# Optimization experiments

Hardware: AMD Instinct MI355X
Metric: run time of the kernel (lower is better)

## Reference

```python
import jax, jax.numpy as jnp
import numpy as np

B, L, D, P = 4, 128, 256, 1024
TU, TB = 86400, 3600  # tu = 24*3600, time_bin = 3600
NEG = float(-2**32 + 1)


def setup_inputs() -> dict:
    key = jax.random.key(0)
    ks = jax.random.split(key, 16)
    src = jax.random.normal(ks[0], (B, L, D), jnp.float32)
    batch_seq_lens = jax.random.randint(ks[1], (B,), L // 2, L + 1, dtype=jnp.int32)
    ts = jnp.sort(jax.random.randint(ks[2], (B, L), 0, 864000, dtype=jnp.int32), axis=1)
    lts = ts + jax.random.randint(ks[3], (B, L), 0, 7200, dtype=jnp.int32)
    s = 0.02
    hour_emb = (jax.random.normal(ks[4], (TU // TB + 2, D), jnp.float32) * s).at[0].set(0.0)  # padding_idx=0
    day_emb = (jax.random.normal(ks[5], (8, D), jnp.float32) * s).at[0].set(0.0)              # padding_idx=0
    wq = jax.random.normal(ks[6], (D, D), jnp.float32) * s
    wk = jax.random.normal(ks[7], (D, D), jnp.float32) * s
    wv = jax.random.normal(ks[8], (D, D), jnp.float32) * s
    wf1 = jax.random.normal(ks[9], (D, D), jnp.float32) * s
    wf2 = jax.random.normal(ks[10], (D, D), jnp.float32) * s
    wdec = jax.random.uniform(ks[11], (P, D), jnp.float32, -0.1, 0.1)  # init_weights uniform(-0.1,0.1)
    z = jnp.zeros((D,), jnp.float32)
    return {
        'src': src, 'hour_emb': hour_emb, 'day_emb': day_emb,
        'wq': wq, 'bq': z, 'wk': wk, 'bk': z, 'wv': wv, 'bv': z,
        'g11': jnp.ones((D,), jnp.float32), 'b11': z,
        'wf1': wf1, 'bf1': z, 'wf2': wf2, 'bf2': z,
        'g12': jnp.ones((D,), jnp.float32), 'b12': z,
        'wdec': wdec, 'bdec': jnp.zeros((P,), jnp.float32),
        'batch_seq_lens': batch_seq_lens,
        'batch_input_seqs_ts': ts,
        'batch_label_seqs_ts': lts,
    }


def _ln(x, g, b):
    m = jnp.mean(x, axis=-1, keepdims=True)
    v = jnp.var(x, axis=-1, keepdims=True)
    return (x - m) * jax.lax.rsqrt(v + 1e-5) * g + b


def reference(src, hour_emb, day_emb, wq, bq, wk, bk, wv, bv, g11, b11,
              wf1, bf1, wf2, bf2, g12, b12, wdec, bdec,
              batch_seq_lens, batch_input_seqs_ts, batch_label_seqs_ts):
    ts, lts = batch_input_seqs_ts, batch_label_seqs_ts
    # per-pair time intervals, [B,L,L]
    diff = ts[:, :, None] - ts[:, None, :]
    hour = (diff % TU) // TB + 2
    # faithful to source: 'if i == j' compares batch index to row position
    hour = jnp.where((jnp.arange(B)[:, None] == jnp.arange(L)[None, :])[:, :, None], 1, hour)
    day = jnp.minimum(diff // TU + 1, 7)
    ldiff = lts[:, :, None] - ts[:, None, :]
    lhour = (ldiff % TU) // TB + 2
    lday = jnp.minimum(ldiff // TU + 1, 7)
    tril = jnp.tril(jnp.ones((L, L), bool))
    rows_valid = jnp.arange(L)[None, :] < batch_seq_lens[:, None]  # [B,L]
    valid = tril[None] & rows_valid[:, :, None]
    # index 0 == padding row (zero embedding), matching zeros-init + padding_idx=0
    hour = jnp.where(valid, hour, 0)
    day = jnp.where(valid, day, 0)
    lhour = jnp.where(valid, lhour, 0)
    lday = jnp.where(valid, lday, 0)
    hE = hour_emb[hour]    # [B,L,L,D]
    dE = day_emb[day]
    lhE = hour_emb[lhour]
    ldE = day_emb[lday]

    Q = src @ wq.T + bq
    K = src @ wk.T + bk
    V = src @ wv.T + bv
    aw = (jnp.einsum('bjd,bkd->bjk', Q, K)
          + jnp.einsum('bjkd,bjd->bjk', hE, Q)
          + jnp.einsum('bjkd,bjd->bjk', dE, Q)) / jnp.sqrt(jnp.float32(D))
    mask = (~tril)[None] | (~rows_valid)[:, :, None]
    aw = jnp.where(mask, NEG, aw)
    aw = jax.nn.softmax(aw, axis=-1)
    x = (jnp.einsum('bjk,bkd->bjd', aw, V)
         + jnp.einsum('bjk,bjkd->bjd', aw, hE)
         + jnp.einsum('bjk,bjkd->bjd', aw, dE))
    x = _ln(x + src, g11, b11)
    f = jnp.maximum(x @ wf1.T + bf1, 0.0) @ wf2.T + bf2  # dropout is identity at eval
    f = _ln(x + f, g12, b12)

    # out4[b,j,k,:] = f[b,k,:] + label interval embeddings
    out4 = f[:, None, :, :] + lhE + ldE            # [B,L,L,D]
    dec = out4 @ wdec.T + bdec                     # [B,L,L,P]
    counts = jnp.arange(1, L + 1, dtype=dec.dtype)
    pooled = jnp.einsum('bjkp,jk->bjp', dec, tril.astype(dec.dtype)) / counts[None, :, None]
    return pooled
```

## Files before the change

### kernel.cpp

```cpp
#include <hip/hip_runtime.h>
#include <hip/hip_bf16.h>

#define LL 128
#define DD 256
#define PP 1024
#define TU_C 86400
#define TB_C 3600
#define NEGF -4294967296.0f

#define FMA4(ACC_, SS_, WW_) { (ACC_).x += (SS_)*(WW_).x; (ACC_).y += (SS_)*(WW_).y; (ACC_).z += (SS_)*(WW_).z; (ACC_).w += (SS_)*(WW_).w; }
#define ADD4(ACC_, WW_) { (ACC_).x += (WW_).x; (ACC_).y += (WW_).y; (ACC_).z += (WW_).z; (ACC_).w += (WW_).w; }

__device__ __forceinline__ float wredSum(float v) {
#pragma unroll
  for (int o = 32; o; o >>= 1) v += __shfl_xor(v, o);
  return v;
}
__device__ __forceinline__ float wredMax(float v) {
#pragma unroll
  for (int o = 32; o; o >>= 1) v = fmaxf(v, __shfl_xor(v, o));
  return v;
}

__global__ __launch_bounds__(256) void k_wt(
    const float* __restrict__ wq, const float* __restrict__ wk,
    const float* __restrict__ wv, const float* __restrict__ wf1,
    const float* __restrict__ wf2, const float* __restrict__ wdec,
    float* __restrict__ wt)
{
  __shared__ float s[32][33];
  const int tile = blockIdx.x;
  const float* src; float* dst; int R, m;
  if (tile < 320) {
    const int mi = tile >> 6; m = tile & 63;
    src = (mi == 0) ? wq : (mi == 1) ? wk : (mi == 2) ? wv : (mi == 3) ? wf1 : wf2;
    dst = wt + mi * 65536; R = 256;
  } else {
    m = tile - 320; src = wdec; dst = wt + 327680; R = 1024;
  }
  const int sr = (m >> 3) * 32, sc0 = (m & 7) * 32;
  const int tx = threadIdx.x & 31, ty = threadIdx.x >> 5;
#pragma unroll
  for (int i = 0; i < 4; ++i)
    s[ty + 8 * i][tx] = src[(sr + ty + 8 * i) * 256 + sc0 + tx];
  __syncthreads();
#pragma unroll
  for (int i = 0; i < 4; ++i)
    dst[(sc0 + ty + 8 * i) * R + sr + tx] = s[tx][ty + 8 * i];
}

__global__ __launch_bounds__(256) void k_qkv(
    const float* __restrict__ src, const float* __restrict__ wt,
    const float* __restrict__ bq, const float* __restrict__ bk,
    const float* __restrict__ bv,
    float* __restrict__ Q, float* __restrict__ KT, float* __restrict__ V)
{
  __shared__ float xs[8][DD];
  __shared__ float ps[4][8][DD];
  const int t = threadIdx.x, l = t & 63, w = t >> 6;
  const int r0 = blockIdx.x * 8;
  const int mat = blockIdx.y;
  const float* wm = wt + mat * 65536;
  for (int i = t; i < 8 * DD; i += 256) xs[i >> 8][i & 255] = src[r0 * DD + i];
  __syncthreads();
  const int col = 4 * l;
  float4 acc[8];
#pragma unroll
  for (int r = 0; r < 8; ++r) acc[r] = (float4){0.f, 0.f, 0.f, 0.f};
  const int e0 = 64 * w;
  for (int e = e0; e < e0 + 64; e += 4) {
    float4 xr[8];
#pragma unroll
    for (int r = 0; r < 8; ++r) xr[r] = *(const float4*)&xs[r][e];
#pragma unroll
    for (int c = 0; c < 4; ++c) {
      const float4 w4 = *(const float4*)(wm + (e + c) * DD + col);
#pragma unroll
      for (int r = 0; r < 8; ++r) {
        const float xv = (c == 0) ? xr[r].x : (c == 1) ? xr[r].y : (c == 2) ? xr[r].z : xr[r].w;
        FMA4(acc[r], xv, w4)
      }
    }
  }
#pragma unroll
  for (int r = 0; r < 8; ++r) *(float4*)&ps[w][r][col] = acc[r];
  __syncthreads();
  const float* bi = (mat == 0) ? bq : (mat == 1) ? bk : bv;
#pragma unroll
  for (int g = 0; g < 2; ++g) {
    const int combo = g * 256 + t;
    const int r = combo >> 6, cgp = combo & 63;
    const int c4 = 4 * cgp;
    float4 o = *(const float4*)(bi + c4);
    ADD4(o, (*(const float4*)&ps[0][r][c4]))
    ADD4(o, (*(const float4*)&ps[1][r][c4]))
    ADD4(o, (*(const float4*)&ps[2][r][c4]))
    ADD4(o, (*(const float4*)&ps[3][r][c4]))
    const int rr = r0 + r;
    if (mat == 1) {
      const int bA = rr >> 7, kA = rr & 127;
      KT[bA * 32768 + (c4 + 0) * 128 + kA] = o.x;
      KT[bA * 32768 + (c4 + 1) * 128 + kA] = o.y;
      KT[bA * 32768 + (c4 + 2) * 128 + kA] = o.z;
      KT[bA * 32768 + (c4 + 3) * 128 + kA] = o.w;
    } else {
      float* op = (mat == 0) ? Q : V;
      *(float4*)(op + rr * DD + c4) = o;
    }
  }
}

__global__ __launch_bounds__(512) void k_attn(
    const float* __restrict__ Q, const float* __restrict__ KT,
    const float* __restrict__ Vm, const float* __restrict__ src,
    const float* __restrict__ hour_emb, const float* __restrict__ day_emb,
    const int* __restrict__ seq_lens, const int* __restrict__ ts_g,
    const float* __restrict__ g11, const float* __restrict__ b11,
    const float* __restrict__ wt1, const float* __restrict__ bf1,
    const float* __restrict__ wt2, const float* __restrict__ bf2,
    const float* __restrict__ g12, const float* __restrict__ b12,
    float* __restrict__ F)
{
  const int b = blockIdx.x >> 6;
  const int j0 = (blockIdx.x & 63) * 2;
  const int t = threadIdx.x, w = t >> 6, l = t & 63;
  const int col = 4 * l;
  __shared__ float qs[2][DD];
  __shared__ int   tsl[LL];
  __shared__ float qhd[2][34];
  __shared__ float whd[2][34];
  __shared__ float red[8];
  __shared__ float ss[2][LL];
  __shared__ float xs2[2][DD];
  __shared__ float hs2[2][DD];
  __shared__ float ps[8][2][DD];
  const int row0 = b * LL + j0;
  qs[t >> 8][t & 255] = Q[row0 * DD + t];
  if (t < LL) tsl[t] = ts_g[b * LL + t];
  if (t < 68) whd[t / 34][t % 34] = 0.f;
  __syncthreads();
  float kdot = 0.f;
  int krow = 0, kidx = 0;
  if (w < 4) {
    krow = w >> 1;
    kidx = ((w & 1) << 6) | l;
    const float* ktb = KT + b * 32768;
    float4 kd = {0.f,0.f,0.f,0.f};
#pragma unroll 8
    for (int e = 0; e < DD; e += 4) {
      const float4 q4 = *(const float4*)&qs[krow][e];
      const float* kp = ktb + e * LL + kidx;
      kd.x += q4.x * kp[0];
      kd.y += q4.y * kp[128];
      kd.z += q4.z * kp[256];
      kd.w += q4.w * kp[384];
    }
    kdot = (kd.x + kd.y) + (kd.z + kd.w);
  } else if (w < 6 && l < 34) {
    const int r = w - 4;
    const float* ep = (l < 26) ? (hour_emb + l * DD) : (day_emb + (l - 26) * DD);
    float4 ed = {0.f,0.f,0.f,0.f};
    for (int e = 0; e < DD; e += 4) {
      const float4 q4 = *(const float4*)&qs[r][e];
      const float4 e4 = *(const float4*)(ep + e);
      ed.x += q4.x * e4.x; ed.y += q4.y * e4.y;
      ed.z += q4.z * e4.z; ed.w += q4.w * e4.w;
    }
    qhd[r][l] = (ed.x + ed.y) + (ed.z + ed.w);
  }
  __syncthreads();
  const int len = seq_lens[b];
  float s = NEGF;
  int hidx = 0, didx = 0;
  if (w < 4) {
    const int jrow = j0 + krow;
    if (kidx <= jrow && jrow < len) {
      const int df = tsl[jrow] - tsl[kidx];
      hidx = (jrow == b) ? 1 : ((df % TU_C) / TB_C + 2);
      didx = min(df / TU_C + 1, 7);
      s = (kdot + qhd[krow][hidx] + qhd[krow][26 + didx]) * 0.0625f;
    }
    const float mv = wredMax(s);
    if (l == 0) red[w] = mv;
  }
  __syncthreads();
  float p = 0.f;
  if (w < 4) {
    const float m = fmaxf(red[2 * krow], red[2 * krow + 1]);
    p = expf(s - m);
    const float sv = wredSum(p);
    if (l == 0) red[4 + w] = sv;
  }
  __syncthreads();
  if (w < 4) {
    const float Z = red[4 + 2 * krow] + red[5 + 2 * krow];
    const float aw = p / Z;
    ss[krow][kidx] = aw;
    atomicAdd(&whd[krow][hidx], aw);
    atomicAdd(&whd[krow][26 + didx], aw);
  }
  __syncthreads();
  {
    float4 a0 = {0.f,0.f,0.f,0.f}, a1 = {0.f,0.f,0.f,0.f};
    const float* vb = Vm + b * LL * DD + col;
    const int k0 = 16 * w;
#pragma unroll
    for (int kk = 0; kk < 16; ++kk) {
      const int k = k0 + kk;
      const float4 v4 = *(const float4*)(vb + k * DD);
      FMA4(a0, ss[0][k], v4)
      FMA4(a1, ss[1][k], v4)
    }
    if (w == 0) {
#pragma unroll
      for (int i = 0; i < 26; ++i)
        FMA4(a0, whd[0][i], *(const float4*)(hour_emb + i * DD + col))
    } else if (w == 1) {
#pragma unroll
      for (int i = 0; i < 26; ++i)
        FMA4(a1, whd[1][i], *(const float4*)(hour_emb + i * DD + col))
    } else if (w == 2) {
#pragma unroll
      for (int i = 0; i < 8; ++i)
        FMA4(a0, whd[0][26 + i], *(const float4*)(day_emb + i * DD + col))
      const float4 s4 = *(const float4*)(src + row0 * DD + col);
      ADD4(a0, s4)
    } else if (w == 3) {
#pragma unroll
      for (int i = 0; i < 8; ++i)
        FMA4(a1, whd[1][26 + i], *(const float4*)(day_emb + i * DD + col))
      const float4 s4 = *(const float4*)(src + (row0 + 1) * DD + col);
      ADD4(a1, s4)
    }
    *(float4*)&ps[w][0][col] = a0;
    *(float4*)&ps[w][1][col] = a1;
  }
  __syncthreads();
  if (w < 2) {
    float4 x = *(const float4*)&ps[0][w][col];
#pragma unroll
    for (int i = 1; i < 8; ++i) ADD4(x, (*(const float4*)&ps[i][w][col]))
    const float sm = wredSum(x.x + x.y + x.z + x.w);
    const float sq = wredSum(x.x*x.x + x.y*x.y + x.z*x.z + x.w*x.w);
    const float mean = sm * (1.f / DD);
    const float rstd = rsqrtf(sq * (1.f / DD) - mean * mean + 1e-5f);
    const float4 g4 = *(const float4*)(g11 + col);
    const float4 b4 = *(const float4*)(b11 + col);
    x.x = (x.x - mean) * rstd * g4.x + b4.x;
    x.y = (x.y - mean) * rstd * g4.y + b4.y;
    x.z = (x.z - mean) * rstd * g4.z + b4.z;
    x.w = (x.w - mean) * rstd * g4.w + b4.w;
    *(float4*)&xs2[w][col] = x;
  }
  __syncthreads();
  {
    float4 a0 = {0.f,0.f,0.f,0.f}, a1 = {0.f,0.f,0.f,0.f};
    const int e0 = 32 * w;
#pragma unroll 8
    for (int ee = 0; ee < 32; ++ee) {
      const int e = e0 + ee;
      const float4 w4 = *(const float4*)(wt1 + e * DD + col);
      FMA4(a0, xs2[0][e], w4)
      FMA4(a1, xs2[1][e], w4)
    }
    *(float4*)&ps[w][0][col] = a0;
    *(float4*)&ps[w][1][col] = a1;
  }
  __syncthreads();
  if (w < 2) {
    float4 h = *(const float4*)(bf1 + col);
#pragma unroll
    for (int i = 0; i < 8; ++i) ADD4(h, (*(const float4*)&ps[i][w][col]))
    h.x = fmaxf(h.x, 0.f); h.y = fmaxf(h.y, 0.f);
    h.z = fmaxf(h.z, 0.f); h.w = fmaxf(h.w, 0.f);
    *(float4*)&hs2[w][col] = h;
  }
  __syncthreads();
  {
    float4 a0 = {0.f,0.f,0.f,0.f}, a1 = {0.f,0.f,0.f,0.f};
    const int e0 = 32 * w;
#pragma unroll 8
    for (int ee = 0; ee < 32; ++ee) {
      const int e = e0 + ee;
      const float4 w4 = *(const float4*)(wt2 + e * DD + col);
      FMA4(a0, hs2[0][e], w4)
      FMA4(a1, hs2[1][e], w4)
    }
    *(float4*)&ps[w][0][col] = a0;
    *(float4*)&ps[w][1][col] = a1;
  }
  __syncthreads();
  if (w < 2) {
    float4 o = *(const float4*)(bf2 + col);
#pragma unroll
    for (int i = 0; i < 8; ++i) ADD4(o, (*(const float4*)&ps[i][w][col]))
    const float4 xr = *(const float4*)&xs2[w][col];
    ADD4(o, xr)
    const float sm = wredSum(o.x + o.y + o.z + o.w);
    const float sq = wredSum(o.x*o.x + o.y*o.y + o.z*o.z + o.w*o.w);
    const float mean = sm * (1.f / DD);
    const float rstd = rsqrtf(sq * (1.f / DD) - mean * mean + 1e-5f);
    const float4 g4 = *(const float4*)(g12 + col);
    const float4 b4 = *(const float4*)(b12 + col);
    o.x = (o.x - mean) * rstd * g4.x + b4.x;
    o.y = (o.y - mean) * rstd * g4.y + b4.y;
    o.z = (o.z - mean) * rstd * g4.z + b4.z;
    o.w = (o.w - mean) * rstd * g4.w + b4.w;
    *(float4*)(F + (row0 + w) * DD + col) = o;
  }
}

__global__ __launch_bounds__(256) void k_decf(
    const float* __restrict__ F,
    const float* __restrict__ hour_emb, const float* __restrict__ day_emb,
    const int* __restrict__ seq_lens, const int* __restrict__ ts_g,
    const int* __restrict__ lts_g,
    const float* __restrict__ wtd, const float* __restrict__ bdec,
    float* __restrict__ out)
{
  const int c0 = blockIdx.x * 256;
  const int r0g = blockIdx.y * 8;
  const int b = r0g >> 7, j0 = r0g & 127;
  const int t = threadIdx.x, l = t & 63, w = t >> 6;
  __shared__ float xs[8][DD];
  __shared__ float cnt[8][34];
  __shared__ float ps[4][8][DD];
  for (int i = t; i < 8 * 34; i += 256) (&cnt[0][0])[i] = 0.f;
  __syncthreads();
  const int len = seq_lens[b];
  const int* ts = ts_g + b * LL;
  const int* lts = lts_g + b * LL;
#pragma unroll
  for (int p = 0; p < 4; ++p) {
    const int idx = p * 256 + t;
    const int jj = idx >> 7, k = idx & 127, j = j0 + jj;
    if (k <= j && j < len) {
      const int ld = lts[j] - ts[k];
      atomicAdd(&cnt[jj][(ld % TU_C) / TB_C + 2], 1.f);
      atomicAdd(&cnt[jj][26 + min(ld / TU_C + 1, 7)], 1.f);
    }
  }
  __syncthreads();
  {
    float he[26], de[8];
#pragma unroll
    for (int i = 0; i < 26; ++i) he[i] = hour_emb[i * DD + t];
#pragma unroll
    for (int i = 0; i < 8; ++i)  de[i] = day_emb[i * DD + t];
    const float* fb = F + b * LL * DD + t;
    float A0 = 0.f, A1 = 0.f, A2 = 0.f, A3 = 0.f;
#pragma unroll 4
    for (int k = 0; k < j0; k += 4) {
      A0 += fb[(k + 0) * DD]; A1 += fb[(k + 1) * DD];
      A2 += fb[(k + 2) * DD]; A3 += fb[(k + 3) * DD];
    }
    float gacc = (A0 + A1) + (A2 + A3);
#pragma unroll
    for (int jj = 0; jj < 8; ++jj) {
      gacc += fb[(j0 + jj) * DD];
      float s0 = 0.f, s1 = 0.f;
#pragma unroll
      for (int i = 0; i < 26; i += 2) {
        s0 += cnt[jj][i] * he[i]; s1 += cnt[jj][i + 1] * he[i + 1];
      }
#pragma unroll
      for (int i = 0; i < 8; i += 2) {
        s0 += cnt[jj][26 + i] * de[i]; s1 += cnt[jj][27 + i] * de[i + 1];
      }
      xs[jj][t] = (gacc + s0 + s1) / (float)(j0 + jj + 1);
    }
  }
  __syncthreads();
  const int col = c0 + 4 * l;
  float4 acc[8];
#pragma unroll
  for (int r = 0; r < 8; ++r) acc[r] = (float4){0.f, 0.f, 0.f, 0.f};
  const int e0 = 64 * w;
  for (int e = e0; e < e0 + 64; e += 4) {
    float4 xr[8];
#pragma unroll
    for (int r = 0; r < 8; ++r) xr[r] = *(const float4*)&xs[r][e];
#pragma unroll
    for (int c = 0; c < 4; ++c) {
      const float4 w4 = *(const float4*)(wtd + (e + c) * PP + col);
#pragma unroll
      for (int r = 0; r < 8; ++r) {
        const float xv = (c == 0) ? xr[r].x : (c == 1) ? xr[r].y : (c == 2) ? xr[r].z : xr[r].w;
        FMA4(acc[r], xv, w4)
      }
    }
  }
#pragma unroll
  for (int r = 0; r < 8; ++r) *(float4*)&ps[w][r][4 * l] = acc[r];
  __syncthreads();
#pragma unroll
  for (int g = 0; g < 2; ++g) {
    const int combo = g * 256 + t;
    const int r = combo >> 6, cgp = combo & 63;
    const int c4 = 4 * cgp;
    float4 o = *(const float4*)(bdec + c0 + c4);
    ADD4(o, (*(const float4*)&ps[0][r][c4]))
    ADD4(o, (*(const float4*)&ps[1][r][c4]))
    ADD4(o, (*(const float4*)&ps[2][r][c4]))
    ADD4(o, (*(const float4*)&ps[3][r][c4]))
    *(float4*)(out + (r0g + r) * PP + c0 + c4) = o;
  }
}

extern "C" void kernel_launch(void* const* d_in, const int* in_sizes, int n_in,
                              void* d_out, int out_size, void* d_ws, size_t ws_size,
                              hipStream_t stream)
{
  (void)in_sizes; (void)n_in; (void)out_size; (void)ws_size;
  const float* src      = (const float*)d_in[0];
  const float* hour_emb = (const float*)d_in[1];
  const float* day_emb  = (const float*)d_in[2];
  const float* wq  = (const float*)d_in[3];
  const float* bq  = (const float*)d_in[4];
  const float* wk  = (const float*)d_in[5];
  const float* bk  = (const float*)d_in[6];
  const float* wv  = (const float*)d_in[7];
  const float* bv  = (const float*)d_in[8];
  const float* g11 = (const float*)d_in[9];
  const float* b11 = (const float*)d_in[10];
  const float* wf1 = (const float*)d_in[11];
  const float* bf1 = (const float*)d_in[12];
  const float* wf2 = (const float*)d_in[13];
  const float* bf2 = (const float*)d_in[14];
  const float* g12 = (const float*)d_in[15];
  const float* b12 = (const float*)d_in[16];
  const float* wdec = (const float*)d_in[17];
  const float* bdec = (const float*)d_in[18];
  const int* seq_lens = (const int*)d_in[19];
  const int* ts  = (const int*)d_in[20];
  const int* lts = (const int*)d_in[21];
  float* out = (float*)d_out;
  float* ws = (float*)d_ws;
  float* WT = ws;
  float* Q  = ws + 589824;
  float* KT = ws + 720896;
  float* V  = ws + 851968;
  float* F  = ws + 983040;

  k_wt  <<<576, 256, 0, stream>>>(wq, wk, wv, wf1, wf2, wdec, WT);
  k_qkv <<<dim3(64, 3), 256, 0, stream>>>(src, WT, bq, bk, bv, Q, KT, V);
  k_attn<<<256, 512, 0, stream>>>(Q, KT, V, src, hour_emb, day_emb, seq_lens, ts,
                                  g11, b11, WT + 196608, bf1, WT + 262144, bf2,
                                  g12, b12, F);
  k_decf<<<dim3(4, 64), 256, 0, stream>>>(F, hour_emb, day_emb, seq_lens, ts, lts,
                                          WT + 327680, bdec, out);
}
```

Before: 50.36 us.

## Merge four kernel launches into one cooperative persistent kernel with grid syncs

Replaces the four separate launches (weight transpose, QKV projection, attention+FFN, decoder pooling) with a single cooperative kernel of 256 blocks × 512 threads. The phases are separated by grid.sync() and share one shared-memory union. The goal is to remove per-launch overhead and inter-kernel gaps. Trade-offs: grid-wide barriers have their own cost, some phases now run on fewer or reshaped blocks (QKV uses 192 blocks with 8 waves splitting K), and the larger union shared footprint may reduce occupancy.

Measured after the change: 152.4 us. +202.6%, slower.

```diff
diff --git a/kernel.cpp b/kernel.cpp
--- a/kernel.cpp
+++ b/kernel.cpp
@@ -1,5 +1,8 @@
 #include <hip/hip_runtime.h>
+#include <hip/hip_cooperative_groups.h>
 #include <hip/hip_bf16.h>
+
+namespace cg = cooperative_groups;
 
 #define LL 128
 #define DD 256
@@ -22,81 +25,117 @@
   return v;
 }
 
-__global__ __launch_bounds__(256) void k_wt(
+struct P0S { float tile[2][32][33]; };
+struct P1S { float xs[8][DD]; float ps[4][8][DD]; };
+struct P2S { float qs[2][DD]; int tsl[LL]; float qhd[2][34]; float whd[2][34];
+             float red[8]; float ss[2][LL]; float xs2[2][DD]; float hs2[2][DD];
+             float ps[8][2][DD]; };
+struct P3S { float xs[8][DD]; float cnt[8][34]; float pa[2][DD]; float ps[4][8][DD]; };
+union SMEM { P0S p0; P1S p1; P2S p2; P3S p3; };
+
+__global__ __launch_bounds__(512) void k_mono(
     const float* __restrict__ wq, const float* __restrict__ wk,
     const float* __restrict__ wv, const float* __restrict__ wf1,
     const float* __restrict__ wf2, const float* __restrict__ wdec,
-    float* __restrict__ wt)
-{
-  __shared__ float s[32][33];
-  const int tile = blockIdx.x;
-  const float* src; float* dst; int R, m;
-  if (tile < 320) {
-    const int mi = tile >> 6; m = tile & 63;
-    src = (mi == 0) ? wq : (mi == 1) ? wk : (mi == 2) ? wv : (mi == 3) ? wf1 : wf2;
-    dst = wt + mi * 65536; R = 256;
-  } else {
-    m = tile - 320; src = wdec; dst = wt + 327680; R = 1024;
-  }
-  const int sr = (m >> 3) * 32, sc0 = (m & 7) * 32;
-  const int tx = threadIdx.x & 31, ty = threadIdx.x >> 5;
-#pragma unroll
-  for (int i = 0; i < 4; ++i)
-    s[ty + 8 * i][tx] = src[(sr + ty + 8 * i) * 256 + sc0 + tx];
-  __syncthreads();
-#pragma unroll
-  for (int i = 0; i < 4; ++i)
-    dst[(sc0 + ty + 8 * i) * R + sr + tx] = s[tx][ty + 8 * i];
-}
-
-__global__ __launch_bounds__(256) void k_qkv(
-    const float* __restrict__ src, const float* __restrict__ wt,
+    const float* __restrict__ src,
+    const float* __restrict__ hour_emb, const float* __restrict__ day_emb,
     const float* __restrict__ bq, const float* __restrict__ bk,
     const float* __restrict__ bv,
-    float* __restrict__ Q, float* __restrict__ KT, float* __restrict__ V)
+    const float* __restrict__ g11, const float* __restrict__ b11,
+    const float* __restrict__ bf1, const float* __restrict__ bf2,
+    const float* __restrict__ g12, const float* __restrict__ b12,
+    const float* __restrict__ bdec,
+    const int* __restrict__ seq_lens, const int* __restrict__ ts_g,
+    const int* __restrict__ lts_g,
+    float* __restrict__ out,
+    float* __restrict__ WT, float* __restrict__ Q, float* __restrict__ KT,
+    float* __restrict__ V, float* __restrict__ F)
 {
-  __shared__ float xs[8][DD];
-  __shared__ float ps[4][8][DD];
-  const int t = threadIdx.x, l = t & 63, w = t >> 6;
-  const int r0 = blockIdx.x * 8;
-  const int mat = blockIdx.y;
-  const float* wm = wt + mat * 65536;
-  for (int i = t; i < 8 * DD; i += 256) xs[i >> 8][i & 255] = src[r0 * DD + i];
-  __syncthreads();
-  const int col = 4 * l;
-  float4 acc[8];
-#pragma unroll
-  for (int r = 0; r < 8; ++r) acc[r] = (float4){0.f, 0.f, 0.f, 0.f};
-  const int e0 = 64 * w;
-  for (int e = e0; e < e0 + 64; e += 4) {
-    float4 xr[8];
-#pragma unroll
-    for (int r = 0; r < 8; ++r) xr[r] = *(const float4*)&xs[r][e];
-#pragma unroll
-    for (int c = 0; c < 4; ++c) {
-      const float4 w4 = *(const float4*)(wm + (e + c) * DD + col);
-#pragma unroll
-      for (int r = 0; r < 8; ++r) {
-        const float xv = (c == 0) ? xr[r].x : (c == 1) ? xr[r].y : (c == 2) ? xr[r].z : xr[r].w;
-        FMA4(acc[r], xv, w4)
+  cg::grid_group grid = cg::this_grid();
+  __shared__ SMEM sm;
+  const int bx = blockIdx.x;
+  const int t = threadIdx.x;
+  const int w = t >> 6, l = t & 63;
+
+  {
+    const int sub = t >> 8, tt = t & 255;
+    const int tx = tt & 31, ty = tt >> 5;
+    for (int base = 0; base < 576; base += 512) {
+      const int tile = base + 2 * bx + sub;
+      __syncthreads();
+      const float* sw = nullptr; float* dst = nullptr; int R = 256, m = 0;
+      if (tile < 576) {
+        if (tile < 320) {
+          const int mi = tile >> 6; m = tile & 63;
+          sw = (mi == 0) ? wq : (mi == 1) ? wk : (mi == 2) ? wv : (mi == 3) ? wf1 : wf2;
+          dst = WT + mi * 65536; R = 256;
+        } else {
+          m = tile - 320; sw = wdec; dst = WT + 327680; R = 1024;
+        }
+        const int sr = (m >> 3) * 32, sc0 = (m & 7) * 32;
+#pragma unroll
+        for (int i = 0; i < 4; ++i)
+          sm.p0.tile[sub][ty + 8 * i][tx] = sw[(sr + ty + 8 * i) * 256 + sc0 + tx];
+      }
+      __syncthreads();
+      if (tile < 576) {
+        const int sr = (m >> 3) * 32, sc0 = (m & 7) * 32;
+#pragma unroll
+        for (int i = 0; i < 4; ++i)
+          dst[(sc0 + ty + 8 * i) * R + sr + tx] = sm.p0.tile[sub][tx][ty + 8 * i];
       }
     }
   }
-#pragma unroll
-  for (int r = 0; r < 8; ++r) *(float4*)&ps[w][r][col] = acc[r];
-  __syncthreads();
-  const float* bi = (mat == 0) ? bq : (mat == 1) ? bk : bv;
-#pragma unroll
-  for (int g = 0; g < 2; ++g) {
-    const int combo = g * 256 + t;
-    const int r = combo >> 6, cgp = combo & 63;
-    const int c4 = 4 * cgp;
+  grid.sync();
+
+  if (bx < 192) {
+    const int mat = bx >> 6;
+    const int r0 = (bx & 63) * 8;
+    for (int i = t; i < 8 * DD; i += 512) sm.p1.xs[i >> 8][i & 255] = src[r0 * DD + i];
+    __syncthreads();
+    const float* wm = WT + mat * 65536;
+    float4 acc[8];
+#pragma unroll
+    for (int r = 0; r < 8; ++r) acc[r] = (float4){0.f, 0.f, 0.f, 0.f};
+    const int e0 = 32 * w;
+    for (int e = e0; e < e0 + 32; e += 4) {
+      float4 xr[8];
+#pragma unroll
+      for (int r = 0; r < 8; ++r) xr[r] = *(const float4*)&sm.p1.xs[r][e];
+#pragma unroll
+      for (int c = 0; c < 4; ++c) {
+        const float4 w4 = *(const float4*)(wm + (e + c) * DD + 4 * l);
+#pragma unroll
+        for (int r = 0; r < 8; ++r) {
+          const float xv = (c == 0) ? xr[r].x : (c == 1) ? xr[r].y : (c == 2) ? xr[r].z : xr[r].w;
+          FMA4(acc[r], xv, w4)
+        }
+      }
+    }
+    if (w < 4) {
+#pragma unroll
+      for (int r = 0; r < 8; ++r) *(float4*)&sm.p1.ps[w][r][4 * l] = acc[r];
+    }
+    __syncthreads();
+    const int orow = t >> 6, c4 = 4 * (t & 63);
+    float4 p1 = *(const float4*)&sm.p1.ps[0][orow][c4];
+    ADD4(p1, (*(const float4*)&sm.p1.ps[1][orow][c4]))
+    ADD4(p1, (*(const float4*)&sm.p1.ps[2][orow][c4]))
+    ADD4(p1, (*(const float4*)&sm.p1.ps[3][orow][c4]))
+    __syncthreads();
+    if (w >= 4) {
+#pragma unroll
+      for (int r = 0; r < 8; ++r) *(float4*)&sm.p1.ps[w - 4][r][4 * l] = acc[r];
+    }
+    __syncthreads();
+    const float* bi = (mat == 0) ? bq : (mat == 1) ? bk : bv;
     float4 o = *(const float4*)(bi + c4);
-    ADD4(o, (*(const float4*)&ps[0][r][c4]))
-    ADD4(o, (*(const float4*)&ps[1][r][c4]))
-    ADD4(o, (*(const float4*)&ps[2][r][c4]))
-    ADD4(o, (*(const float4*)&ps[3][r][c4]))
-    const int rr = r0 + r;
+    ADD4(o, p1)
+    ADD4(o, (*(const float4*)&sm.p1.ps[0][orow][c4]))
+    ADD4(o, (*(const float4*)&sm.p1.ps[1][orow][c4]))
+    ADD4(o, (*(const float4*)&sm.p1.ps[2][orow][c4]))
+    ADD4(o, (*(const float4*)&sm.p1.ps[3][orow][c4]))
+    const int rr = r0 + orow;
     if (mat == 1) {
       const int bA = rr >> 7, kA = rr & 127;
       KT[bA * 32768 + (c4 + 0) * 128 + kA] = o.x;
@@ -108,302 +147,288 @@
       *(float4*)(op + rr * DD + c4) = o;
     }
   }
-}
-
-__global__ __launch_bounds__(512) void k_attn(
-    const float* __restrict__ Q, const float* __restrict__ KT,
-    const float* __restrict__ Vm, const float* __restrict__ src,
-    const float* __restrict__ hour_emb, const float* __restrict__ day_emb,
-    const int* __restrict__ seq_lens, const int* __restrict__ ts_g,
-    const float* __restrict__ g11, const float* __restrict__ b11,
-    const float* __restrict__ wt1, const float* __restrict__ bf1,
-    const float* __restrict__ wt2, const float* __restrict__ bf2,
-    const float* __restrict__ g12, const float* __restrict__ b12,
-    float* __restrict__ F)
-{
-  const int b = blockIdx.x >> 6;
-  const int j0 = (blockIdx.x & 63) * 2;
-  const int t = threadIdx.x, w = t >> 6, l = t & 63;
-  const int col = 4 * l;
-  __shared__ float qs[2][DD];
-  __shared__ int   tsl[LL];
-  __shared__ float qhd[2][34];
-  __shared__ float whd[2][34];
-  __shared__ float red[8];
-  __shared__ float ss[2][LL];
-  __shared__ float xs2[2][DD];
-  __shared__ float hs2[2][DD];
-  __shared__ float ps[8][2][DD];
-  const int row0 = b * LL + j0;
-  qs[t >> 8][t & 255] = Q[row0 * DD + t];
-  if (t < LL) tsl[t] = ts_g[b * LL + t];
-  if (t < 68) whd[t / 34][t % 34] = 0.f;
-  __syncthreads();
-  float kdot = 0.f;
-  int krow = 0, kidx = 0;
-  if (w < 4) {
-    krow = w >> 1;
-    kidx = ((w & 1) << 6) | l;
-    const float* ktb = KT + b * 32768;
-    float4 kd = {0.f,0.f,0.f,0.f};
+  grid.sync();
+
+  {
+    const int b = bx >> 6;
+    const int j0 = (bx & 63) * 2;
+    const int col = 4 * l;
+    const int row0 = b * LL + j0;
+    sm.p2.qs[t >> 8][t & 255] = Q[row0 * DD + t];
+    if (t < LL) sm.p2.tsl[t] = ts_g[b * LL + t];
+    if (t < 68) sm.p2.whd[t / 34][t % 34] = 0.f;
+    __syncthreads();
+    float kdot = 0.f;
+    int krow = 0, kidx = 0;
+    if (w < 4) {
+      krow = w >> 1;
+      kidx = ((w & 1) << 6) | l;
+      const float* ktb = KT + b * 32768;
+      float4 kd = {0.f,0.f,0.f,0.f};
 #pragma unroll 8
-    for (int e = 0; e < DD; e += 4) {
-      const float4 q4 = *(const float4*)&qs[krow][e];
-      const float* kp = ktb + e * LL + kidx;
-      kd.x += q4.x * kp[0];
-      kd.y += q4.y * kp[128];
-      kd.z += q4.z * kp[256];
-      kd.w += q4.w * kp[384];
-    }
-    kdot = (kd.x + kd.y) + (kd.z + kd.w);
-  } else if (w < 6 && l < 34) {
-    const int r = w - 4;
-    const float* ep = (l < 26) ? (hour_emb + l * DD) : (day_emb + (l - 26) * DD);
-    float4 ed = {0.f,0.f,0.f,0.f};
-    for (int e = 0; e < DD; e += 4) {
-      const float4 q4 = *(const float4*)&qs[r][e];
-      const float4 e4 = *(const float4*)(ep + e);
-      ed.x += q4.x * e4.x; ed.y += q4.y * e4.y;
-      ed.z += q4.z * e4.z; ed.w += q4.w * e4.w;
-    }
-    qhd[r][l] = (ed.x + ed.y) + (ed.z + ed.w);
+      for (int e = 0; e < DD; e += 4) {
+        const float4 q4 = *(const float4*)&sm.p2.qs[krow][e];
+        const float* kp = ktb + e * LL + kidx;
+        kd.x += q4.x * kp[0];
+        kd.y += q4.y * kp[128];
+        kd.z += q4.z * kp[256];
+        kd.w += q4.w * kp[384];
+      }
+      kdot = (kd.x + kd.y) + (kd.z + kd.w);
+    } else if (w < 6 && l < 34) {
+      const int r = w - 4;
+      const float* ep = (l < 26) ? (hour_emb + l * DD) : (day_emb + (l - 26) * DD);
+      float4 ed = {0.f,0.f,0.f,0.f};
+      for (int e = 0; e < DD; e += 4) {
+        const float4 q4 = *(const float4*)&sm.p2.qs[r][e];
+        const float4 e4 = *(const float4*)(ep + e);
+        ed.x += q4.x * e4.x; ed.y += q4.y * e4.y;
+        ed.z += q4.z * e4.z; ed.w += q4.w * e4.w;
+      }
+      sm.p2.qhd[r][l] = (ed.x + ed.y) + (ed.z + ed.w);
+    }
+    __syncthreads();
+    const int len = seq_lens[b];
+    float s = NEGF;
+    int hidx = 0, didx = 0;
+    if (w < 4) {
+      const int jrow = j0 + krow;
+      if (kidx <= jrow && jrow < len) {
+        const int df = sm.p2.tsl[jrow] - sm.p2.tsl[kidx];
+        hidx = (jrow == b) ? 1 : ((df % TU_C) / TB_C + 2);
+        didx = min(df / TU_C + 1, 7);
+        s = (kdot + sm.p2.qhd[krow][hidx] + sm.p2.qhd[krow][26 + didx]) * 0.0625f;
+      }
+      const float mv = wredMax(s);
+      if (l == 0) sm.p2.red[w] = mv;
+    }
+    __syncthreads();
+    float p = 0.f;
+    if (w < 4) {
+      const float m = fmaxf(sm.p2.red[2 * krow], sm.p2.red[2 * krow + 1]);
+      p = expf(s - m);
+      const float sv = wredSum(p);
+      if (l == 0) sm.p2.red[4 + w] = sv;
+    }
+    __syncthreads();
+    if (w < 4) {
+      const float Z = sm.p2.red[4 + 2 * krow] + sm.p2.red[5 + 2 * krow];
+      const float aw = p / Z;
+      sm.p2.ss[krow][kidx] = aw;
+      atomicAdd(&sm.p2.whd[krow][hidx], aw);
+      atomicAdd(&sm.p2.whd[krow][26 + didx], aw);
+    }
+    __syncthreads();
+    {
+      float4 a0 = {0.f,0.f,0.f,0.f}, a1 = {0.f,0.f,0.f,0.f};
+      const float* vb = V + b * LL * DD + col;
+      const int k0 = 16 * w;
+#pragma unroll
+      for (int kk = 0; kk < 16; ++kk) {
+        const int k = k0 + kk;
+        const float4 v4 = *(const float4*)(vb + k * DD);
+        FMA4(a0, sm.p2.ss[0][k], v4)
+        FMA4(a1, sm.p2.ss[1][k], v4)
+      }
+      if (w == 0) {
+#pragma unroll
+        for (int i = 0; i < 26; ++i)
+          FMA4(a0, sm.p2.whd[0][i], *(const float4*)(hour_emb + i * DD + col))
+      } else if (w == 1) {
+#pragma unroll
+        for (int i = 0; i < 26; ++i)
+          FMA4(a1, sm.p2.whd[1][i], *(const float4*)(hour_emb + i * DD + col))
+      } else if (w == 2) {
+#pragma unroll
+        for (int i = 0; i < 8; ++i)
+          FMA4(a0, sm.p2.whd[0][26 + i], *(const float4*)(day_emb + i * DD + col))
+        const float4 s4 = *(const float4*)(src + row0 * DD + col);
+        ADD4(a0, s4)
+      } else if (w == 3) {
+#pragma unroll
+        for (int i = 0; i < 8; ++i)
+          FMA4(a1, sm.p2.whd[1][26 + i], *(const float4*)(day_emb + i * DD + col))
+        const float4 s4 = *(const float4*)(src + (row0 + 1) * DD + col);
+        ADD4(a1, s4)
+      }
+      *(float4*)&sm.p2.ps[w][0][col] = a0;
+      *(float4*)&sm.p2.ps[w][1][col] = a1;
+    }
+    __syncthreads();
+    if (w < 2) {
+      float4 x = *(const float4*)&sm.p2.ps[0][w][col];
+#pragma unroll
+      for (int i = 1; i < 8; ++i) ADD4(x, (*(const float4*)&sm.p2.ps[i][w][col]))
+      const float smv = wredSum(x.x + x.y + x.z + x.w);
+      const float sq = wredSum(x.x*x.x + x.y*x.y + x.z*x.z + x.w*x.w);
+      const float mean = smv * (1.f / DD);
+      const float rstd = rsqrtf(sq * (1.f / DD) - mean * mean + 1e-5f);
+      const float4 g4 = *(const float4*)(g11 + col);
+      const float4 b4 = *(const float4*)(b11 + col);
+      x.x = (x.x - mean) * rstd * g4.x + b4.x;
+      x.y = (x.y - mean) * rstd * g4.y + b4.y;
+      x.z = (x.z - mean) * rstd * g4.z + b4.z;
+      x.w = (x.w - mean) * rstd * g4.w + b4.w;
+      *(float4*)&sm.p2.xs2[w][col] = x;
+    }
+    __syncthreads();
+    {
+      float4 a0 = {0.f,0.f,0.f,0.f}, a1 = {0.f,0.f,0.f,0.f};
+      const float* wt1 = WT + 196608;
+      const int e0 = 32 * w;
+#pragma unroll 8
+      for (int ee = 0; ee < 32; ++ee) {
+        const int e = e0 + ee;
+        const float4 w4 = *(const float4*)(wt1 + e * DD + col);
+        FMA4(a0, sm.p2.xs2[0][e], w4)
+        FMA4(a1, sm.p2.xs2[1][e], w4)
+      }
+      *(float4*)&sm.p2.ps[w][0][col] = a0;
+      *(float4*)&sm.p2.ps[w][1][col] = a1;
+    }
+    __syncthreads();
+    if (w < 2) {
+      float4 h = *(const float4*)(bf1 + col);
+#pragma unroll
+      for (int i = 0; i < 8; ++i) ADD4(h, (*(const float4*)&sm.p2.ps[i][w][col]))
+      h.x = fmaxf(h.x, 0.f); h.y = fmaxf(h.y, 0.f);
+      h.z = fmaxf(h.z, 0.f); h.w = fmaxf(h.w, 0.f);
+      *(float4*)&sm.p2.hs2[w][col] = h;
+    }
+    __syncthreads();
+    {
+      float4 a0 = {0.f,0.f,0.f,0.f}, a1 = {0.f,0.f,0.f,0.f};
+      const float* wt2 = WT + 262144;
+      const int e0 = 32 * w;
+#pragma unroll 8
+      for (int ee = 0; ee < 32; ++ee) {
+        const int e = e0 + ee;
+        const float4 w4 = *(const float4*)(wt2 + e * DD + col);
+        FMA4(a0, sm.p2.hs2[0][e], w4)
+        FMA4(a1, sm.p2.hs2[1][e], w4)
+      }
+      *(float4*)&sm.p2.ps[w][0][col] = a0;
+      *(float4*)&sm.p2.ps[w][1][col] = a1;
+    }
+    __syncthreads();
+    if (w < 2) {
+      float4 o = *(const float4*)(bf2 + col);
+#pragma unroll
+      for (int i = 0; i < 8; ++i) ADD4(o, (*(const float4*)&sm.p2.ps[i][w][col]))
+      const float4 xr = *(const float4*)&sm.p2.xs2[w][col];
+      ADD4(o, xr)
+      const float smv = wredSum(o.x + o.y + o.z + o.w);
+      const float sq = wredSum(o.x*o.x + o.y*o.y + o.z*o.z + o.w*o.w);
+      const float mean = smv * (1.f / DD);
+      const float rstd = rsqrtf(sq * (1.f / DD) - mean * mean + 1e-5f);
+      const float4 g4 = *(const float4*)(g12 + col);
+      const float4 b4 = *(const float4*)(b12 + col);
+      o.x = (o.x - mean) * rstd * g4.x + b4.x;
+      o.y = (o.y - mean) * rstd * g4.y + b4.y;
+      o.z = (o.z - mean) * rstd * g4.z + b4.z;
+      o.w = (o.w - mean) * rstd * g4.w + b4.w;
+      *(float4*)(F + (row0 + w) * DD + col) = o;
+    }
   }
-  __syncthreads();
-  const int len = seq_lens[b];
-  float s = NEGF;
-  int hidx = 0, didx = 0;
-  if (w < 4) {
-    const int jrow = j0 + krow;
-    if (kidx <= jrow && jrow < len) {
-      const int df = tsl[jrow] - tsl[kidx];
-      hidx = (jrow == b) ? 1 : ((df % TU_C) / TB_C + 2);
-      didx = min(df / TU_C + 1, 7);
-      s = (kdot + qhd[krow][hidx] + qhd[krow][26 + didx]) * 0.0625f;
-    }
-    const float mv = wredMax(s);
-    if (l == 0) red[w] = mv;
-  }
-  __syncthreads();
-  float p = 0.f;
-  if (w < 4) {
-    const float m = fmaxf(red[2 * krow], red[2 * krow + 1]);
-    p = expf(s - m);
-    const float sv = wredSum(p);
-    if (l == 0) red[4 + w] = sv;
-  }
-  __syncthreads();
-  if (w < 4) {
-    const float Z = red[4 + 2 * krow] + red[5 + 2 * krow];
-    const float aw = p / Z;
-    ss[krow][kidx] = aw;
-    atomicAdd(&whd[krow][hidx], aw);
-    atomicAdd(&whd[krow][26 + didx], aw);
-  }
-  __syncthreads();
+  grid.sync();
+
   {
-    float4 a0 = {0.f,0.f,0.f,0.f}, a1 = {0.f,0.f,0.f,0.f};
-    const float* vb = Vm + b * LL * DD + col;
-    const int k0 = 16 * w;
-#pragma unroll
-    for (int kk = 0; kk < 16; ++kk) {
-      const int k = k0 + kk;
-      const float4 v4 = *(const float4*)(vb + k * DD);
-      FMA4(a0, ss[0][k], v4)
-      FMA4(a1, ss[1][k], v4)
-    }
-    if (w == 0) {
-#pragma unroll
-      for (int i = 0; i < 26; ++i)
-        FMA4(a0, whd[0][i], *(const float4*)(hour_emb + i * DD + col))
-    } else if (w == 1) {
-#pragma unroll
-      for (int i = 0; i < 26; ++i)
-        FMA4(a1, whd[1][i], *(const float4*)(hour_emb + i * DD + col))
-    } else if (w == 2) {
-#pragma unroll
-      for (int i = 0; i < 8; ++i)
-        FMA4(a0, whd[0][26 + i], *(const float4*)(day_emb + i * DD + col))
-      const float4 s4 = *(const float4*)(src + row0 * DD + col);
-      ADD4(a0, s4)
-    } else if (w == 3) {
-#pragma unroll
-      for (int i = 0; i < 8; ++i)
-        FMA4(a1, whd[1][26 + i], *(const float4*)(day_emb + i * DD + col))
-      const float4 s4 = *(const float4*)(src + (row0 + 1) * DD + col);
-      ADD4(a1, s4)
-    }
-    *(float4*)&ps[w][0][col] = a0;
-    *(float4*)&ps[w][1][col] = a1;
-  }
-  __syncthreads();
-  if (w < 2) {
-    float4 x = *(const float4*)&ps[0][w][col];
-#pragma unroll
-    for (int i = 1; i < 8; ++i) ADD4(x, (*(const float4*)&ps[i][w][col]))
-    const float sm = wredSum(x.x + x.y + x.z + x.w);
-    const float sq = wredSum(x.x*x.x + x.y*x.y + x.z*x.z + x.w*x.w);
-    const float mean = sm * (1.f / DD);
-    const float rstd = rsqrtf(sq * (1.f / DD) - mean * mean + 1e-5f);
-    const float4 g4 = *(const float4*)(g11 + col);
-    const float4 b4 = *(const float4*)(b11 + col);
-    x.x = (x.x - mean) * rstd * g4.x + b4.x;
-    x.y = (x.y - mean) * rstd * g4.y + b4.y;
-    x.z = (x.z - mean) * rstd * g4.z + b4.z;
-    x.w = (x.w - mean) * rstd * g4.w + b4.w;
-    *(float4*)&xs2[w][col] = x;
-  }
-  __syncthreads();
-  {
-    float4 a0 = {0.f,0.f,0.f,0.f}, a1 = {0.f,0.f,0.f,0.f};
+    const int c0 = (bx & 3) * 256;
+    const int r0g = (bx >> 2) * 8;
+    const int b = r0g >> 7, j0 = r0g & 127;
+    for (int i = t; i < 8 * 34; i += 512) (&sm.p3.cnt[0][0])[i] = 0.f;
+    __syncthreads();
+    const int len = seq_lens[b];
+    const int* ts = ts_g + b * LL;
+    const int* lts = lts_g + b * LL;
+#pragma unroll
+    for (int pp = 0; pp < 2; ++pp) {
+      const int idx = pp * 512 + t;
+      const int jj = idx >> 7, k = idx & 127, j = j0 + jj;
+      if (k <= j && j < len) {
+        const int ld = lts[j] - ts[k];
+        atomicAdd(&sm.p3.cnt[jj][(ld % TU_C) / TB_C + 2], 1.f);
+        atomicAdd(&sm.p3.cnt[jj][26 + min(ld / TU_C + 1, 7)], 1.f);
+      }
+    }
+    {
+      const int g = t >> 8, d = t & 255;
+      const int kb = (j0 >> 1) * g, ke = (j0 >> 1) * (g + 1);
+      const float* fb = F + b * LL * DD + d;
+      float A0 = 0.f, A1 = 0.f, A2 = 0.f, A3 = 0.f;
+      for (int k = kb; k + 4 <= ke; k += 4) {
+        A0 += fb[(k + 0) * DD]; A1 += fb[(k + 1) * DD];
+        A2 += fb[(k + 2) * DD]; A3 += fb[(k + 3) * DD];
+      }
+      sm.p3.pa[g][d] = (A0 + A1) + (A2 + A3);
+    }
+    __syncthreads();
+    if (t < 256) {
+      float he[26], de[8];
+#pragma unroll
+      for (int i = 0; i < 26; ++i) he[i] = hour_emb[i * DD + t];
+#pragma unroll
+      for (int i = 0; i < 8; ++i)  de[i] = day_emb[i * DD + t];
+      const float* fb = F + b * LL * DD + t;
+      float gacc = sm.p3.pa[0][t] + sm.p3.pa[1][t];
+#pragma unroll
+      for (int jj = 0; jj < 8; ++jj) {
+        gacc += fb[(j0 + jj) * DD];
+        float s0 = 0.f, s1 = 0.f;
+#pragma unroll
+        for (int i = 0; i < 26; i += 2) {
+          s0 += sm.p3.cnt[jj][i] * he[i]; s1 += sm.p3.cnt[jj][i + 1] * he[i + 1];
+        }
+#pragma unroll
+        for (int i = 0; i < 8; i += 2) {
+          s0 += sm.p3.cnt[jj][26 + i] * de[i]; s1 += sm.p3.cnt[jj][27 + i] * de[i + 1];
+        }
+        sm.p3.xs[jj][t] = (gacc + s0 + s1) / (float)(j0 + jj + 1);
+      }
+    }
+    __syncthreads();
+    const float* wtd = WT + 327680;
+    float4 acc[8];
+#pragma unroll
+    for (int r = 0; r < 8; ++r) acc[r] = (float4){0.f, 0.f, 0.f, 0.f};
     const int e0 = 32 * w;
-#pragma unroll 8
-    for (int ee = 0; ee < 32; ++ee) {
-      const int e = e0 + ee;
-      const float4 w4 = *(const float4*)(wt1 + e * DD + col);
-      FMA4(a0, xs2[0][e], w4)
-      FMA4(a1, xs2[1][e], w4)
-    }
-    *(float4*)&ps[w][0][col] = a0;
-    *(float4*)&ps[w][1][col] = a1;
-  }
-  __syncthreads();
-  if (w < 2) {
-    float4 h = *(const float4*)(bf1 + col);
-#pragma unroll
-    for (int i = 0; i < 8; ++i) ADD4(h, (*(const float4*)&ps[i][w][col]))
-    h.x = fmaxf(h.x, 0.f); h.y = fmaxf(h.y, 0.f);
-    h.z = fmaxf(h.z, 0.f); h.w = fmaxf(h.w, 0.f);
-    *(float4*)&hs2[w][col] = h;
-  }
-  __syncthreads();
-  {
-    float4 a0 = {0.f,0.f,0.f,0.f}, a1 = {0.f,0.f,0.f,0.f};
-    const int e0 = 32 * w;
-#pragma unroll 8
-    for (int ee = 0; ee < 32; ++ee) {
-      const int e = e0 + ee;
-      const float4 w4 = *(const float4*)(wt2 + e * DD + col);
-      FMA4(a0, hs2[0][e], w4)
-      FMA4(a1, hs2[1][e], w4)
-    }
-    *(float4*)&ps[w][0][col] = a0;
-    *(float4*)&ps[w][1][col] = a1;
-  }
-  __syncthreads();
-  if (w < 2) {
-    float4 o = *(const float4*)(bf2 + col);
-#pragma unroll
-    for (int i = 0; i < 8; ++i) ADD4(o, (*(const float4*)&ps[i][w][col]))
-    const float4 xr = *(const float4*)&xs2[w][col];
-    ADD4(o, xr)
-    const float sm = wredSum(o.x + o.y + o.z + o.w);
-    const float sq = wredSum(o.x*o.x + o.y*o.y + o.z*o.z + o.w*o.w);
-    const float mean = sm * (1.f / DD);
-    const float rstd = rsqrtf(sq * (1.f / DD) - mean * mean + 1e-5f);
-    const float4 g4 = *(const float4*)(g12 + col);
-    const float4 b4 = *(const float4*)(b12 + col);
-    o.x = (o.x - mean) * rstd * g4.x + b4.x;
-    o.y = (o.y - mean) * rstd * g4.y + b4.y;
-    o.z = (o.z - mean) * rstd * g4.z + b4.z;
-    o.w = (o.w - mean) * rstd * g4.w + b4.w;
-    *(float4*)(F + (row0 + w) * DD + col) = o;
-  }
-}
-
-__global__ __launch_bounds__(256) void k_decf(
-    const float* __restrict__ F,
-    const float* __restrict__ hour_emb, const float* __restrict__ day_emb,
-    const int* __restrict__ seq_lens, const int* __restrict__ ts_g,
-    const int* __restrict__ lts_g,
-    const float* __restrict__ wtd, const float* __restrict__ bdec,
-    float* __restrict__ out)
-{
-  const int c0 = blockIdx.x * 256;
-  const int r0g = blockIdx.y * 8;
-  const int b = r0g >> 7, j0 = r0g & 127;
-  const int t = threadIdx.x, l = t & 63, w = t >> 6;
-  __shared__ float xs[8][DD];
-  __shared__ float cnt[8][34];
-  __shared__ float ps[4][8][DD];
-  for (int i = t; i < 8 * 34; i += 256) (&cnt[0][0])[i] = 0.f;
-  __syncthreads();
-  const int len = seq_lens[b];
-  const int* ts = ts_g + b * LL;
-  const int* lts = lts_g + b * LL;
-#pragma unroll
-  for (int p = 0; p < 4; ++p) {
-    const int idx = p * 256 + t;
-    const int jj = idx >> 7, k = idx & 127, j = j0 + jj;
-    if (k <= j && j < len) {
-      const int ld = lts[j] - ts[k];
-      atomicAdd(&cnt[jj][(ld % TU_C) / TB_C + 2], 1.f);
-      atomicAdd(&cnt[jj][26 + min(ld / TU_C + 1, 7)], 1.f);
-    }
-  }
-  __syncthreads();
-  {
-    float he[26], de[8];
-#pragma unroll
-    for (int i = 0; i < 26; ++i) he[i] = hour_emb[i * DD + t];
-#pragma unroll
-    for (int i = 0; i < 8; ++i)  de[i] = day_emb[i * DD + t];
-    const float* fb = F + b * LL * DD + t;
-    float A0 = 0.f, A1 = 0.f, A2 = 0.f, A3 = 0.f;
-#pragma unroll 4
-    for (int k = 0; k < j0; k += 4) {
-      A0 += fb[(k + 0) * DD]; A1 += fb[(k + 1) * DD];
-      A2 += fb[(k + 2) * DD]; A3 += fb[(k + 3) * DD];
-    }
-    float gacc = (A0 + A1) + (A2 + A3);
-#pragma unroll
-    for (int jj = 0; jj < 8; ++jj) {
-      gacc += fb[(j0 + jj) * DD];
-      float s0 = 0.f, s1 = 0.f;
-#pragma unroll
-      for (int i = 0; i < 26; i += 2) {
-        s0 += cnt[jj][i] * he[i]; s1 += cnt[jj][i + 1] * he[i + 1];
-      }
-#pragma unroll
-      for (int i = 0; i < 8; i += 2) {
-        s0 += cnt[jj][26 + i] * de[i]; s1 += cnt[jj][27 + i] * de[i + 1];
-      }
-      xs[jj][t] = (gacc + s0 + s1) / (float)(j0 + jj + 1);
-    }
-  }
-  __syncthreads();
-  const int col = c0 + 4 * l;
-  float4 acc[8];
-#pragma unroll
-  for (int r = 0; r < 8; ++r) acc[r] = (float4){0.f, 0.f, 0.f, 0.f};
-  const int e0 = 64 * w;
-  for (int e = e0; e < e0 + 64; e += 4) {
-    float4 xr[8];
-#pragma unroll
-    for (int r = 0; r < 8; ++r) xr[r] = *(const float4*)&xs[r][e];
-#pragma unroll
-    for (int c = 0; c < 4; ++c) {
-      const float4 w4 = *(const float4*)(wtd + (e + c) * PP + col);
-#pragma unroll
-      for (int r = 0; r < 8; ++r) {
-        const float xv = (c == 0) ? xr[r].x : (c == 1) ? xr[r].y : (c == 2) ? xr[r].z : xr[r].w;
-        FMA4(acc[r], xv, w4)
-      }
-    }
-  }
-#pragma unroll
-  for (int r = 0; r < 8; ++r) *(float4*)&ps[w][r][4 * l] = acc[r];
-  __syncthreads();
-#pragma unroll
-  for (int g = 0; g < 2; ++g) {
-    const int combo = g * 256 + t;
-    const int r = combo >> 6, cgp = combo & 63;
-    const int c4 = 4 * cgp;
+    for (int e = e0; e < e0 + 32; e += 4) {
+      float4 xr[8];
+#pragma unroll
+      for (int r = 0; r < 8; ++r) xr[r] = *(const float4*)&sm.p3.xs[r][e];
+#pragma unroll
+      for (int c = 0; c < 4; ++c) {
+        const float4 w4 = *(const float4*)(wtd + (e + c) * PP + c0 + 4 * l);
+#pragma unroll
+        for (int r = 0; r < 8; ++r) {
+          const float xv = (c == 0) ? xr[r].x : (c == 1) ? xr[r].y : (c == 2) ? xr[r].z : xr[r].w;
+          FMA4(acc[r], xv, w4)
+        }
+      }
+    }
+    if (w < 4) {
+#pragma unroll
+      for (int r = 0; r < 8; ++r) *(float4*)&sm.p3.ps[w][r][4 * l] = acc[r];
+    }
+    __syncthreads();
+    const int orow = t >> 6, c4 = 4 * (t & 63);
+    float4 p1 = *(const float4*)&sm.p3.ps[0][orow][c4];
+    ADD4(p1, (*(const float4*)&sm.p3.ps[1][orow][c4]))
+    ADD4(p1, (*(const float4*)&sm.p3.ps[2][orow][c4]))
+    ADD4(p1, (*(const float4*)&sm.p3.ps[3][orow][c4]))
+    __syncthreads();
+    if (w >= 4) {
+#pragma unroll
+      for (int r = 0; r < 8; ++r) *(float4*)&sm.p3.ps[w - 4][r][4 * l] = acc[r];
+    }
+    __syncthreads();
     float4 o = *(const float4*)(bdec + c0 + c4);
-    ADD4(o, (*(const float4*)&ps[0][r][c4]))
-    ADD4(o, (*(const float4*)&ps[1][r][c4]))
-    ADD4(o, (*(const float4*)&ps[2][r][c4]))
-    ADD4(o, (*(const float4*)&ps[3][r][c4]))
-    *(float4*)(out + (r0g + r) * PP + c0 + c4) = o;
+    ADD4(o, p1)
+    ADD4(o, (*(const float4*)&sm.p3.ps[0][orow][c4]))
+    ADD4(o, (*(const float4*)&sm.p3.ps[1][orow][c4]))
+    ADD4(o, (*(const float4*)&sm.p3.ps[2][orow][c4]))
+    ADD4(o, (*(const float4*)&sm.p3.ps[3][orow][c4]))
+    *(float4*)(out + (r0g + orow) * PP + c0 + c4) = o;
   }
 }
 
@@ -442,11 +467,14 @@
   float* V  = ws + 851968;
   float* F  = ws + 983040;
 
-  k_wt  <<<576, 256, 0, stream>>>(wq, wk, wv, wf1, wf2, wdec, WT);
-  k_qkv <<<dim3(64, 3), 256, 0, stream>>>(src, WT, bq, bk, bv, Q, KT, V);
-  k_attn<<<256, 512, 0, stream>>>(Q, KT, V, src, hour_emb, day_emb, seq_lens, ts,
-                                  g11, b11, WT + 196608, bf1, WT + 262144, bf2,
-                                  g12, b12, F);
-  k_decf<<<dim3(4, 64), 256, 0, stream>>>(F, hour_emb, day_emb, seq_lens, ts, lts,
-                                          WT + 327680, bdec, out);
+  void* args[] = {
+    (void*)&wq, (void*)&wk, (void*)&wv, (void*)&wf1, (void*)&wf2, (void*)&wdec,
+    (void*)&src, (void*)&hour_emb, (void*)&day_emb,
+    (void*)&bq, (void*)&bk, (void*)&bv,
+    (void*)&g11, (void*)&b11, (void*)&bf1, (void*)&bf2, (void*)&g12, (void*)&b12,
+    (void*)&bdec, (void*)&seq_lens, (void*)&ts, (void*)&lts,
+    (void*)&out, (void*)&WT, (void*)&Q, (void*)&KT, (void*)&V, (void*)&F
+  };
+  hipLaunchCooperativeKernel((const void*)k_mono, dim3(256), dim3(512),
+                             args, 0, stream);
 }
```
